# Optimization experiments

Measured on AMD Instinct MI355X. Metric: run time of the kernel, lower is better.

The kernel has to match this reference:

```python
import jax, jax.numpy as jnp
import numpy as np

BETA = 0.25


def setup_inputs() -> dict:
    key = jax.random.key(0)
    k1, k2 = jax.random.split(key)
    z = jax.random.normal(k1, (16, 2048, 64), dtype=jnp.float32)
    emb = jax.random.uniform(k2, (8192, 64), dtype=jnp.float32)  # uniform_() init
    return {"z": z, "emb": emb}


def reference(z, emb):
    # z: [B, N, D], emb: [K, D]; use_norm=False so norm is identity.
    B, N, D = z.shape
    zf = z.reshape(-1, D)                                   # [B*N, D]
    # Squared euclidean distances; argmin is identical to cdist(p=2) argmin.
    d2 = (
        jnp.sum(zf * zf, axis=1, keepdims=True)
        - 2.0 * (zf @ emb.T)
        + jnp.sum(emb * emb, axis=1)
    )                                                       # [B*N, K]
    idx = jnp.argmin(d2, axis=1)                            # [B*N]
    z_q = emb[idx].reshape(z.shape)                         # [B, N, D]
    loss = BETA * jnp.mean((jax.lax.stop_gradient(z_q) - z) ** 2) + jnp.mean(
        (z_q - jax.lax.stop_gradient(z)) ** 2
    )
    z_q_st = z + jax.lax.stop_gradient(z_q - z)             # straight-through
    return z_q_st, idx, loss
```

## Files before the change

### kernel.cpp

```cpp
#include <hip/hip_runtime.h>
#include <hip/hip_bf16.h>
#include <math.h>

#define D 64
#define K_CODES 8192
#define M_QUERIES 32768
#define SLICES 8
#define CODES_PER_SLICE (K_CODES / SLICES)
#define CHUNK 32
#define NCHUNK (CODES_PER_SLICE / CHUNK)
#define QPB 128
#define TAU_V 4e-3f

typedef __attribute__((ext_vector_type(8))) short bf16x8;
typedef __attribute__((ext_vector_type(4))) float f32x4;
typedef __attribute__((ext_vector_type(16))) float f32x16;

__device__ __forceinline__ unsigned short f2bf(float x) {
    __hip_bfloat16 h = __float2bfloat16(x);
    return *reinterpret_cast<unsigned short*>(&h);
}
__device__ __forceinline__ float bf2f(unsigned short s) {
    __hip_bfloat16 h;
    *reinterpret_cast<unsigned short*>(&h) = s;
    return __bfloat162float(h);
}
__device__ __forceinline__ void gld_lds16(const void* g, void* l) {
    __builtin_amdgcn_global_load_lds(
        (const __attribute__((address_space(1))) void*)g,
        (__attribute__((address_space(3))) void*)l, 16, 0, 0);
}
__device__ __forceinline__ void gld_lds4(const void* g, void* l) {
    __builtin_amdgcn_global_load_lds(
        (const __attribute__((address_space(1))) void*)g,
        (__attribute__((address_space(3))) void*)l, 4, 0, 0);
}

__global__ __launch_bounds__(256) void k0_split(const float* __restrict__ emb,
                                                unsigned short* __restrict__ e_hi,
                                                unsigned short* __restrict__ e_lo,
                                                float* __restrict__ halfee,
                                                double* __restrict__ eed,
                                                float* __restrict__ emb_T,
                                                int* __restrict__ ws_cnt,
                                                float* __restrict__ loss_ptr) {
    const int t = threadIdx.x;
    const int grp = blockIdx.x;
    if (grp == 0 && t == 0) { *ws_cnt = 0; *loss_ptr = 0.0f; }
    const int u = t & 7;
#pragma unroll
    for (int it = 0; it < 2; ++it) {
        const int r = (t >> 3) + it * 32;
        const int code = grp * 64 + r;
        const float* src = emb + ((size_t)code * 64 + u * 8);
        float4 f0 = *(const float4*)(src);
        float4 f1 = *(const float4*)(src + 4);
        float f[8] = {f0.x, f0.y, f0.z, f0.w, f1.x, f1.y, f1.z, f1.w};
        bf16x8 h, lo;
        float s = 0.f;
        double sd = 0.0;
#pragma unroll
        for (int j = 0; j < 8; ++j) {
            float e = f[j];
            s += e * e;
            sd += (double)e * (double)e;
            unsigned short hh = f2bf(e);
            h[j]  = (short)hh;
            lo[j] = (short)f2bf(e - bf2f(hh));
        }
        const int c32 = code >> 5, r32 = code & 31;
        size_t off = (size_t)c32 * 4096 + (size_t)(u * 32 + r32) * 16;
        *(bf16x8*)((char*)e_hi + off) = h;
        *(bf16x8*)((char*)e_lo + off) = lo;
        s += __shfl_xor(s, 1);
        s += __shfl_xor(s, 2);
        s += __shfl_xor(s, 4);
        sd += __shfl_xor(sd, 1);
        sd += __shfl_xor(sd, 2);
        sd += __shfl_xor(sd, 4);
        if (u == 0) {
            halfee[code] = 0.5f * s + 128.0f;
            eed[code]    = sd;
        }
    }
    {
        const int cl = t & 63;
        const int qd = t >> 6;
        const int code = grp * 64 + cl;
        const int g = code >> 8, cmod = code & 255;
#pragma unroll
        for (int j = 0; j < 16; ++j) {
            int k = qd * 16 + j;
            emb_T[((size_t)g * 64 + k) * 256 + cmod] = emb[(size_t)code * 64 + k];
        }
    }
}

__global__ __launch_bounds__(256, 4) void k1_mfma(const float* __restrict__ z,
                                                  const unsigned short* __restrict__ e_hi,
                                                  const unsigned short* __restrict__ e_lo,
                                                  const float* __restrict__ halfee,
                                                  float4* __restrict__ ws_part) {
    __shared__ __align__(16) unsigned short ldshi[2][CHUNK * 64];
    __shared__ __align__(16) unsigned short ldslo[2][CHUNK * 64];
    __shared__ __align__(16) float ldshe[2][CHUNK];

    const int tid = threadIdx.x;
    const int wid = tid >> 6;
    const int l   = tid & 63;
    const int col = l & 31;
    const int hi  = l >> 5;
    const int slice = blockIdx.y;
    const int chunk0 = slice * NCHUNK;
    const int cbase0 = slice * CODES_PER_SLICE;

    const int qw0 = blockIdx.x * QPB + wid * 32;
    const int qrow = qw0 + col;
    bf16x8 qh[4], ql[4];
    float szz = 0.f;
#pragma unroll
    for (int kk = 0; kk < 4; ++kk) {
        const float* src = z + (size_t)qrow * D + kk * 16 + hi * 8;
        float4 f0 = *(const float4*)(src);
        float4 f1 = *(const float4*)(src + 4);
        float f[8] = {f0.x, f0.y, f0.z, f0.w, f1.x, f1.y, f1.z, f1.w};
        bf16x8 h, lo;
#pragma unroll
        for (int j = 0; j < 8; ++j) {
            szz += f[j] * f[j];
            float x = -f[j];
            unsigned short hh = f2bf(x);
            float r = x - bf2f(hh);
            h[j]  = (short)hh;
            lo[j] = (short)f2bf(r);
        }
        qh[kk] = h;
        ql[kk] = lo;
    }
    szz += __shfl_xor(szz, 32);

    float g1 = 1e30f, g2 = 1e30f;
    int   gi = 0x7fffffff;

#define STAGE(buf, c1)                                                           \
    {                                                                            \
        size_t cb = (size_t)(chunk0 + (c1)) * 4096 + wid * 1024 + l * 16;        \
        gld_lds16((const char*)e_hi + cb, (char*)&ldshi[buf][0] + wid * 1024);   \
        gld_lds16((const char*)e_lo + cb, (char*)&ldslo[buf][0] + wid * 1024);   \
        if (tid < 32)                                                            \
            gld_lds4((const char*)halfee + (size_t)(chunk0 + (c1)) * 128 + tid * 4, \
                     (char*)&ldshe[buf][0]);                                     \
    }

#define MFMA_CHUNK(bufc, acc)                                                    \
    {                                                                            \
        const char*  bh  = (const char*)ldshi[bufc];                             \
        const char*  bl  = (const char*)ldslo[bufc];                             \
        const float* bhe = ldshe[bufc];                                          \
        _Pragma("unroll") for (int g4 = 0; g4 < 4; ++g4) {                       \
            f32x4 he4 = *(const f32x4*)(bhe + g4 * 8 + 4 * hi);                  \
            _Pragma("unroll") for (int j = 0; j < 4; ++j)                        \
                acc[g4 * 4 + j] = he4[j];                                        \
        }                                                                        \
        _Pragma("unroll") for (int kk = 0; kk < 4; ++kk) {                       \
            int a0 = ((kk * 2 + hi) * 32 + col) * 16;                            \
            bf16x8 ah = *(const bf16x8*)(bh + a0);                               \
            bf16x8 al = *(const bf16x8*)(bl + a0);                               \
            acc = __builtin_amdgcn_mfma_f32_32x32x16_bf16(ah, qh[kk], acc, 0, 0, 0); \
            acc = __builtin_amdgcn_mfma_f32_32x32x16_bf16(ah, ql[kk], acc, 0, 0, 0); \
            acc = __builtin_amdgcn_mfma_f32_32x32x16_bf16(al, qh[kk], acc, 0, 0, 0); \
        }                                                                        \
    }

#define TOP2T(acc, cbase)                                                        \
    {                                                                            \
        float t1[8], t2[8];                                                      \
        _Pragma("unroll") for (int i = 0; i < 8; ++i) {                          \
            float va = __int_as_float((__float_as_int(acc[2 * i])     & 0xFFFFFFF0) | (2 * i));     \
            float vb = __int_as_float((__float_as_int(acc[2 * i + 1]) & 0xFFFFFFF0) | (2 * i + 1)); \
            t1[i] = fminf(va, vb);                                               \
            t2[i] = fmaxf(va, vb);                                               \
        }                                                                        \
        _Pragma("unroll") for (int s = 4; s > 0; s >>= 1) {                      \
            _Pragma("unroll") for (int i = 0; i < s; ++i) {                      \
                float m2c = fminf(t2[i], t2[i + s]);                             \
                t2[i] = __builtin_amdgcn_fmed3f(t1[i], t1[i + s], m2c);          \
                t1[i] = fminf(t1[i], t1[i + s]);                                 \
            }                                                                    \
        }                                                                        \
        float m1p = t1[0], m2p = t2[0];                                          \
        int p1 = __float_as_int(m1p) & 15;                                       \
        int code = (cbase) + (p1 & 3) + 8 * (p1 >> 2) + 4 * hi;                  \
        bool lt = m1p < g1;                                                      \
        g2 = fminf(lt ? g1 : g2, lt ? m2p : m1p);                                \
        g1 = lt ? m1p : g1;                                                      \
        gi = lt ? code : gi;                                                     \
    }

    f32x16 accE, accO;

    STAGE(0, 0);
    __syncthreads();
    STAGE(1, 1);
    MFMA_CHUNK(0, accE);
    __syncthreads();
    for (int cc = 1; cc + 1 < NCHUNK; cc += 2) {
        STAGE(0, cc + 1);
        MFMA_CHUNK(1, accO);
        TOP2T(accE, cbase0 + (cc - 1) * CHUNK);
        __syncthreads();
        if (cc + 2 < NCHUNK) STAGE(1, cc + 2);
        MFMA_CHUNK(0, accE);
        TOP2T(accO, cbase0 + cc * CHUNK);
        __syncthreads();
    }
    MFMA_CHUNK(1, accO);
    TOP2T(accE, cbase0 + (NCHUNK - 2) * CHUNK);
    TOP2T(accO, cbase0 + (NCHUNK - 1) * CHUNK);

    {
        float o1 = __shfl_xor(g1, 32);
        float o2 = __shfl_xor(g2, 32);
        int   oi = __shfl_xor(gi, 32);
        bool  take = (o1 < g1) || (o1 == g1 && oi < gi);
        float n2   = take ? fminf(o2, g1) : fminf(g2, o1);
        g1 = take ? o1 : g1;
        gi = take ? oi : gi;
        g2 = n2;
        if (l < 32) {
            int q = qw0 + col;
            ws_part[(size_t)q * SLICES + slice] =
                make_float4(g1, g2, __int_as_float(gi), szz);
        }
    }
#undef STAGE
#undef MFMA_CHUNK
#undef TOP2T
}

__global__ __launch_bounds__(256) void k1b_merge(const float4* __restrict__ ws_part,
                                                 int* __restrict__ ws_idx,
                                                 int* __restrict__ ws_cnt,
                                                 int* __restrict__ ws_list,
                                                 float* __restrict__ out,
                                                 float* __restrict__ loss_ptr) {
    __shared__ float sb[256];
    const int tid = threadIdx.x;
    const int q = blockIdx.x * 256 + tid;
    float m1 = 1e30f, m2 = 1e30f, zz = 0.f;
    int   i1 = 0x7fffffff;
#pragma unroll
    for (int s = 0; s < SLICES; ++s) {
        float4 p = ws_part[(size_t)q * SLICES + s];
        float v1 = p.x, v2 = p.y;
        int   vi = __float_as_int(p.z);
        zz = p.w;
        if (v1 < m1 || (v1 == m1 && vi < i1)) { m2 = fminf(m1, v2); m1 = v1; i1 = vi; }
        else                                  { m2 = fminf(m2, v1); }
    }
    ws_idx[q] = i1;
    out[(size_t)M_QUERIES * D + q] = (float)i1;
    sb[tid] = zz + 2.0f * (m1 - 128.0f);
    if (m2 - m1 < TAU_V) {
        int r = atomicAdd(ws_cnt, 1);
        ws_list[r] = q;
    }
    __syncthreads();
    for (int s = 128; s > 0; s >>= 1) {
        if (tid < s) sb[tid] += sb[tid + s];
        __syncthreads();
    }
    if (tid == 0)
        atomicAdd(loss_ptr, sb[0] * (1.25f / (float)((size_t)M_QUERIES * D)));
}

__global__ __launch_bounds__(256) void k2_rescue(const float* __restrict__ z,
                                                 const float* __restrict__ emb_T,
                                                 const double* __restrict__ eed,
                                                 const int* __restrict__ ws_cnt,
                                                 const int* __restrict__ ws_list,
                                                 int* __restrict__ ws_idx,
                                                 float* __restrict__ out) {
    __shared__ float  zrow[D];
    __shared__ double rv[256];
    __shared__ int    ri[256];
    const int tid = threadIdx.x;
    const int cnt = *ws_cnt;
    for (int r = blockIdx.x; r < cnt; r += gridDim.x) {
        const int q = ws_list[r];
        __syncthreads();
        if (tid < D) zrow[tid] = z[(size_t)q * D + tid];
        __syncthreads();
        double best = 1e300;
        int    bi   = 0x7fffffff;
        for (int g = 0; g < K_CODES / 256; ++g) {
            const float* base = emb_T + (size_t)g * 64 * 256 + tid;
            double d0 = 0.0, d1 = 0.0, d2 = 0.0, d3 = 0.0;
#pragma unroll
            for (int k = 0; k < 64; k += 4) {
                d0 += (double)zrow[k + 0] * (double)base[(size_t)(k + 0) * 256];
                d1 += (double)zrow[k + 1] * (double)base[(size_t)(k + 1) * 256];
                d2 += (double)zrow[k + 2] * (double)base[(size_t)(k + 2) * 256];
                d3 += (double)zrow[k + 3] * (double)base[(size_t)(k + 3) * 256];
            }
            int c = g * 256 + tid;
            double s = fma(-2.0, (d0 + d1) + (d2 + d3), eed[c]);
            if (s < best) { best = s; bi = c; }
        }
        rv[tid] = best;
        ri[tid] = bi;
        __syncthreads();
        for (int s = 128; s > 0; s >>= 1) {
            if (tid < s) {
                double ov = rv[tid + s];
                int    oi = ri[tid + s];
                if (ov < rv[tid] || (ov == rv[tid] && oi < ri[tid])) {
                    rv[tid] = ov;
                    ri[tid] = oi;
                }
            }
            __syncthreads();
        }
        if (tid == 0) {
            ws_idx[q] = ri[0];
            out[(size_t)M_QUERIES * D + q] = (float)ri[0];
        }
        __syncthreads();
    }
}

__global__ __launch_bounds__(256) void k3_gather(const float* __restrict__ emb,
                                                 const int* __restrict__ ws_idx,
                                                 float* __restrict__ out) {
    int g4 = blockIdx.x * 256 + threadIdx.x;
    int q  = g4 >> 4;
    int dd = g4 & 15;
    int id = ws_idx[q];
    float4 v = ((const float4*)(emb + (size_t)id * D))[dd];
    ((float4*)out)[g4] = v;
}

extern "C" void kernel_launch(void* const* d_in, const int* in_sizes, int n_in,
                              void* d_out, int out_size, void* d_ws, size_t ws_size,
                              hipStream_t stream) {
    const float* z   = (const float*)d_in[0];
    const float* emb = (const float*)d_in[1];
    float* out = (float*)d_out;
    char*  ws  = (char*)d_ws;

    unsigned short* e_hi    = (unsigned short*)(ws);
    unsigned short* e_lo    = (unsigned short*)(ws + 1048576);
    float*          halfee  = (float*)(ws + 2097152);
    double*         eed     = (double*)(ws + 2129920);
    float*          emb_T   = (float*)(ws + 2195456);
    float4*         ws_part = (float4*)(ws + 2195456 + 2097152);
    int*            ws_idx  = (int*)(ws + 2195456 + 6291456);
    int*            ws_cnt  = (int*)(ws + 2195456 + 6291456 + 131072);
    int*            ws_list = (int*)(ws + 2195456 + 6291456 + 131136);

    float* loss_ptr = out + (size_t)M_QUERIES * D + M_QUERIES;

    k0_split<<<K_CODES / 64, 256, 0, stream>>>(emb, e_hi, e_lo, halfee, eed,
                                               emb_T, ws_cnt, loss_ptr);

    dim3 g1(M_QUERIES / QPB, SLICES);
    k1_mfma<<<g1, 256, 0, stream>>>(z, e_hi, e_lo, halfee, ws_part);

    k1b_merge<<<M_QUERIES / 256, 256, 0, stream>>>(ws_part, ws_idx, ws_cnt,
                                                   ws_list, out, loss_ptr);

    k2_rescue<<<256, 256, 0, stream>>>(z, emb_T, eed, ws_cnt, ws_list, ws_idx, out);

    k3_gather<<<(M_QUERIES * D / 4) / 256, 256, 0, stream>>>(emb, ws_idx, out);
}
```

Measured before the change: 206.3 us.

## Fuse gather into merge kernel, drop emb transpose and separate gather launch

Removes the transposed codebook copy built in k0_split; the rescue kernel now reads row-major emb directly with float4 loads. The final gather of z_q rows moves into k1b_merge using the block's indices held in shared memory, and rescued queries rewrite their own output row inside k2_rescue. This removes one kernel launch and the transpose writes, at the cost of uncoalesced per-thread row reads in the rescue loop. Correctness depends on k2 overwriting rows after k1b, which stream ordering guarantees.

```diff
diff --git a/kernel.cpp b/kernel.cpp
--- a/kernel.cpp
+++ b/kernel.cpp
@@ -41,7 +41,6 @@
                                                 unsigned short* __restrict__ e_lo,
                                                 float* __restrict__ halfee,
                                                 double* __restrict__ eed,
-                                                float* __restrict__ emb_T,
                                                 int* __restrict__ ws_cnt,
                                                 float* __restrict__ loss_ptr) {
     const int t = threadIdx.x;
@@ -81,17 +80,6 @@
         if (u == 0) {
             halfee[code] = 0.5f * s + 128.0f;
             eed[code]    = sd;
-        }
-    }
-    {
-        const int cl = t & 63;
-        const int qd = t >> 6;
-        const int code = grp * 64 + cl;
-        const int g = code >> 8, cmod = code & 255;
-#pragma unroll
-        for (int j = 0; j < 16; ++j) {
-            int k = qd * 16 + j;
-            emb_T[((size_t)g * 64 + k) * 256 + cmod] = emb[(size_t)code * 64 + k];
         }
     }
 }
@@ -239,12 +227,14 @@
 }
 
 __global__ __launch_bounds__(256) void k1b_merge(const float4* __restrict__ ws_part,
+                                                 const float* __restrict__ emb,
                                                  int* __restrict__ ws_idx,
                                                  int* __restrict__ ws_cnt,
                                                  int* __restrict__ ws_list,
                                                  float* __restrict__ out,
                                                  float* __restrict__ loss_ptr) {
     __shared__ float sb[256];
+    __shared__ int   sidx[256];
     const int tid = threadIdx.x;
     const int q = blockIdx.x * 256 + tid;
     float m1 = 1e30f, m2 = 1e30f, zz = 0.f;
@@ -259,6 +249,7 @@
         else                                  { m2 = fminf(m2, v1); }
     }
     ws_idx[q] = i1;
+    sidx[tid] = i1;
     out[(size_t)M_QUERIES * D + q] = (float)i1;
     sb[tid] = zz + 2.0f * (m1 - 128.0f);
     if (m2 - m1 < TAU_V) {
@@ -272,10 +263,22 @@
     }
     if (tid == 0)
         atomicAdd(loss_ptr, sb[0] * (1.25f / (float)((size_t)M_QUERIES * D)));
+
+    const float4* emb4 = (const float4*)emb;
+    float4*       out4 = (float4*)out;
+    const size_t  base4 = (size_t)blockIdx.x * 256 * 16;
+#pragma unroll
+    for (int i = 0; i < 16; ++i) {
+        int g4l = tid + i * 256;
+        int ql  = g4l >> 4;
+        int dd  = g4l & 15;
+        int id  = sidx[ql];
+        out4[base4 + g4l] = emb4[(size_t)id * 16 + dd];
+    }
 }
 
 __global__ __launch_bounds__(256) void k2_rescue(const float* __restrict__ z,
-                                                 const float* __restrict__ emb_T,
+                                                 const float* __restrict__ emb,
                                                  const double* __restrict__ eed,
                                                  const int* __restrict__ ws_cnt,
                                                  const int* __restrict__ ws_list,
@@ -293,18 +296,18 @@
         __syncthreads();
         double best = 1e300;
         int    bi   = 0x7fffffff;
-        for (int g = 0; g < K_CODES / 256; ++g) {
-            const float* base = emb_T + (size_t)g * 64 * 256 + tid;
-            double d0 = 0.0, d1 = 0.0, d2 = 0.0, d3 = 0.0;
-#pragma unroll
-            for (int k = 0; k < 64; k += 4) {
-                d0 += (double)zrow[k + 0] * (double)base[(size_t)(k + 0) * 256];
-                d1 += (double)zrow[k + 1] * (double)base[(size_t)(k + 1) * 256];
-                d2 += (double)zrow[k + 2] * (double)base[(size_t)(k + 2) * 256];
-                d3 += (double)zrow[k + 3] * (double)base[(size_t)(k + 3) * 256];
+        for (int c = tid; c < K_CODES; c += 256) {
+            const float4* er = (const float4*)(emb + (size_t)c * D);
+            double dot = 0.0;
+#pragma unroll
+            for (int k = 0; k < 16; ++k) {
+                float4 e = er[k];
+                dot += (double)zrow[4 * k + 0] * (double)e.x
+                     + (double)zrow[4 * k + 1] * (double)e.y
+                     + (double)zrow[4 * k + 2] * (double)e.z
+                     + (double)zrow[4 * k + 3] * (double)e.w;
             }
-            int c = g * 256 + tid;
-            double s = fma(-2.0, (d0 + d1) + (d2 + d3), eed[c]);
+            double s = fma(-2.0, dot, eed[c]);
             if (s < best) { best = s; bi = c; }
         }
         rv[tid] = best;
@@ -321,23 +324,15 @@
             }
             __syncthreads();
         }
+        const int fid = ri[0];
         if (tid == 0) {
-            ws_idx[q] = ri[0];
-            out[(size_t)M_QUERIES * D + q] = (float)ri[0];
-        }
-        __syncthreads();
-    }
-}
-
-__global__ __launch_bounds__(256) void k3_gather(const float* __restrict__ emb,
-                                                 const int* __restrict__ ws_idx,
-                                                 float* __restrict__ out) {
-    int g4 = blockIdx.x * 256 + threadIdx.x;
-    int q  = g4 >> 4;
-    int dd = g4 & 15;
-    int id = ws_idx[q];
-    float4 v = ((const float4*)(emb + (size_t)id * D))[dd];
-    ((float4*)out)[g4] = v;
+            ws_idx[q] = fid;
+            out[(size_t)M_QUERIES * D + q] = (float)fid;
+        }
+        if (tid < D)
+            out[(size_t)q * D + tid] = emb[(size_t)fid * D + tid];
+        __syncthreads();
+    }
 }
 
 extern "C" void kernel_launch(void* const* d_in, const int* in_sizes, int n_in,
@@ -352,24 +347,21 @@
     unsigned short* e_lo    = (unsigned short*)(ws + 1048576);
     float*          halfee  = (float*)(ws + 2097152);
     double*         eed     = (double*)(ws + 2129920);
-    float*          emb_T   = (float*)(ws + 2195456);
-    float4*         ws_part = (float4*)(ws + 2195456 + 2097152);
-    int*            ws_idx  = (int*)(ws + 2195456 + 6291456);
-    int*            ws_cnt  = (int*)(ws + 2195456 + 6291456 + 131072);
-    int*            ws_list = (int*)(ws + 2195456 + 6291456 + 131136);
+    float4*         ws_part = (float4*)(ws + 2195456);
+    int*            ws_idx  = (int*)(ws + 2195456 + 4194304);
+    int*            ws_cnt  = (int*)(ws + 2195456 + 4194304 + 131072);
+    int*            ws_list = (int*)(ws + 2195456 + 4194304 + 131136);
 
     float* loss_ptr = out + (size_t)M_QUERIES * D + M_QUERIES;
 
     k0_split<<<K_CODES / 64, 256, 0, stream>>>(emb, e_hi, e_lo, halfee, eed,
-                                               emb_T, ws_cnt, loss_ptr);
+                                               ws_cnt, loss_ptr);
 
     dim3 g1(M_QUERIES / QPB, SLICES);
     k1_mfma<<<g1, 256, 0, stream>>>(z, e_hi, e_lo, halfee, ws_part);
 
-    k1b_merge<<<M_QUERIES / 256, 256, 0, stream>>>(ws_part, ws_idx, ws_cnt,
+    k1b_merge<<<M_QUERIES / 256, 256, 0, stream>>>(ws_part, emb, ws_idx, ws_cnt,
                                                    ws_list, out, loss_ptr);
 
-    k2_rescue<<<256, 256, 0, stream>>>(z, emb_T, eed, ws_cnt, ws_list, ws_idx, out);
-
-    k3_gather<<<(M_QUERIES * D / 4) / 256, 256, 0, stream>>>(emb, ws_idx, out);
-}
+    k2_rescue<<<256, 256, 0, stream>>>(z, emb, eed, ws_cnt, ws_list, ws_idx, out);
+}
```

Result: faster. 181.2 us (-12.2%).
